# Kernel tuning notes

Hardware: AMD Instinct MI355X
Metric: run time of the kernel (lower is better)

## Reference

```python
import jax, jax.numpy as jnp
import numpy as np

N = 50000       # nodes
E = 800000      # edges (avg degree 16)
H = 64          # hidden_channels
T = 4           # towers
F = H // T      # per-tower channels (divide_input=True) = 16
NAGG, NSC = 5, 3
# degree histogram passed as mol_deg -> avg log-degree scaler constant (as in PyG PNAConv)
MOL_DEG = np.array([0, 5, 15, 30, 25, 15, 7, 2, 1], dtype=np.float64)
_bins = np.arange(len(MOL_DEG))
AVG_LOG = float((np.log(_bins + 1.0) * MOL_DEG).sum() / MOL_DEG.sum())


def setup_inputs() -> dict:
    key = jax.random.key(0)
    ks = jax.random.split(key, 12)
    g = lambda k, shp, s=0.1: jax.random.normal(k, shp, dtype=jnp.float32) * s
    return {
        "atom_x": g(ks[0], (N, H), 1.0),
        "bond_emb": g(ks[1], (5, H)),                      # Embedding(5, H)
        "edge_w": g(ks[2], (H, F)), "edge_b": jnp.zeros((F,), jnp.float32),
        "pre_w1": g(ks[3], (T, 3 * F, F)), "pre_b1": jnp.zeros((T, F), jnp.float32),
        "pre_w2": g(ks[4], (T, F, F)), "pre_b2": jnp.zeros((T, F), jnp.float32),
        "post_w1": g(ks[5], (T, (1 + NAGG * NSC) * F, F)), "post_b1": jnp.zeros((T, F), jnp.float32),
        "post_w2": g(ks[6], (T, F, F)), "post_b2": jnp.zeros((T, F), jnp.float32),
        "lin_w": g(ks[7], (H, H)), "lin_b": jnp.zeros((H,), jnp.float32),
        "ln_g": jnp.ones((H,), jnp.float32), "ln_b": jnp.zeros((H,), jnp.float32),
        "bond_x": jax.random.randint(ks[8], (E,), 0, 5),
        "atom_edge_index": jax.random.randint(ks[9], (2, E), 0, N),
    }


def reference(atom_x, bond_emb, edge_w, edge_b, pre_w1, pre_b1, pre_w2, pre_b2,
              post_w1, post_b1, post_w2, post_b2, lin_w, lin_b, ln_g, ln_b,
              bond_x, atom_edge_index):
    src, dst = atom_edge_index[0], atom_edge_index[1]
    # bond encoder + PNA edge encoder (edge_dim -> F_in)
    e = bond_emb[bond_x] @ edge_w + edge_b                       # [E, F]
    xt = atom_x.reshape(N, T, F)                                 # divide_input
    x_j, x_i = xt[src], xt[dst]                                  # [E, T, F]
    et = jnp.broadcast_to(e[:, None, :], (E, T, F))
    h = jnp.concatenate([x_i, x_j, et], axis=-1)                 # [E, T, 3F]
    # per-tower pre-MLP (Linear -> ReLU -> Linear)
    h = jax.nn.relu(jnp.einsum('etf,tfg->etg', h, pre_w1) + pre_b1)
    h = jnp.einsum('etf,tfg->etg', h, pre_w2) + pre_b2           # messages [E, T, F]

    s = jax.ops.segment_sum(h, dst, num_segments=N)
    cnt = jax.ops.segment_sum(jnp.ones((E,), h.dtype), dst, num_segments=N)
    cnt_c = jnp.maximum(cnt, 1.0)[:, None, None]
    mean = s / cnt_c
    mean2 = jax.ops.segment_sum(h * h, dst, num_segments=N) / cnt_c
    std = jnp.sqrt(jax.nn.relu(mean2 - mean * mean) + 1e-5)
    has = (cnt > 0)[:, None, None]
    mn = jnp.where(has, jax.ops.segment_min(h, dst, num_segments=N), 0.0)
    mx = jnp.where(has, jax.ops.segment_max(h, dst, num_segments=N), 0.0)
    agg = jnp.concatenate([s, mean, mn, mx, std], axis=-1)       # [N, T, 5F]

    # degree scalers (deg clamped to 1, as in PyG DegreeScalerAggregation)
    ld = jnp.log(jnp.maximum(cnt, 1.0) + 1.0)[:, None, None]
    agg = jnp.concatenate([agg, agg * (ld / AVG_LOG), agg * (AVG_LOG / ld)], axis=-1)  # [N, T, 15F]

    out = jnp.concatenate([xt, agg], axis=-1)                    # [N, T, 16F]
    # per-tower post-MLP, then mix towers with final Linear
    out = jax.nn.relu(jnp.einsum('ntf,tfg->ntg', out, post_w1) + post_b1)
    out = jnp.einsum('ntf,tfg->ntg', out, post_w2) + post_b2     # [N, T, F]
    out = out.reshape(N, H) @ lin_w + lin_b                      # [N, H]

    # LayerNorm + ReLU + residual (dropout is identity in eval)
    mu = out.mean(-1, keepdims=True)
    var = out.var(-1, keepdims=True)
    ln = (out - mu) / jnp.sqrt(var + 1e-5) * ln_g + ln_b
    return atom_x + jax.nn.relu(ln)
```

## Files before the change

### kernel.cpp

```cpp
#include <hip/hip_runtime.h>
#include <cstdint>

typedef unsigned short u16;
typedef _Float16 half4v __attribute__((ext_vector_type(4)));
typedef float f32x4 __attribute__((ext_vector_type(4)));

#define AVG_LOG_F 1.4862356961977451f
#define MAXD 64

#define OFF_W2   3072
#define OFF_PW1  4096
#define OFF_PW2  20480
#define OFF_LW   21504
#define OFF_PB1  25600
#define OFF_PB2  25664
#define OFF_QB1  25728
#define OFF_QB2  25792
#define OFF_LB   25856
#define OFF_LG   25920
#define OFF_LBN  25984
#define OFF_EWT  26128
#define IB       26448

__device__ __forceinline__ float bf2f(u16 u) {
    return __uint_as_float(((unsigned)u) << 16);
}
__device__ __forceinline__ u16 f2bf(float f) {
    unsigned u = __float_as_uint(f);
    u += 0x7fffu + ((u >> 16) & 1u);
    return (u16)(u >> 16);
}
__device__ __forceinline__ float rdin(const void* p, long j, int mode) {
    if (mode == 0) return bf2f(((const u16*)p)[j]);
    return ((const float*)p)[j];
}
template <int MODE>
__device__ __forceinline__ void load16c(const void* p, long base, float* o) {
    if (MODE == 0) {
        const u16* q = (const u16*)p + base;
        uint4 a = *(const uint4*)q;
        uint4 b = *(const uint4*)(q + 8);
        o[0]  = __uint_as_float(a.x << 16); o[1]  = __uint_as_float(a.x & 0xffff0000u);
        o[2]  = __uint_as_float(a.y << 16); o[3]  = __uint_as_float(a.y & 0xffff0000u);
        o[4]  = __uint_as_float(a.z << 16); o[5]  = __uint_as_float(a.z & 0xffff0000u);
        o[6]  = __uint_as_float(a.w << 16); o[7]  = __uint_as_float(a.w & 0xffff0000u);
        o[8]  = __uint_as_float(b.x << 16); o[9]  = __uint_as_float(b.x & 0xffff0000u);
        o[10] = __uint_as_float(b.y << 16); o[11] = __uint_as_float(b.y & 0xffff0000u);
        o[12] = __uint_as_float(b.z << 16); o[13] = __uint_as_float(b.z & 0xffff0000u);
        o[14] = __uint_as_float(b.w << 16); o[15] = __uint_as_float(b.w & 0xffff0000u);
    } else {
        const float* q = (const float*)p + base;
        float4 a = *(const float4*)q;
        float4 b = *(const float4*)(q + 4);
        float4 c = *(const float4*)(q + 8);
        float4 d = *(const float4*)(q + 12);
        o[0]=a.x; o[1]=a.y; o[2]=a.z; o[3]=a.w;
        o[4]=b.x; o[5]=b.y; o[6]=b.z; o[7]=b.w;
        o[8]=c.x; o[9]=c.y; o[10]=c.z; o[11]=c.w;
        o[12]=d.x; o[13]=d.y; o[14]=d.z; o[15]=d.w;
    }
}

template <int MODE>
__device__ __forceinline__ void y_loop(const void* ax, const void* pre_w1, float* wsY, float* wsXW,
                                       int Nn, int wave, int nwaves, int l) {
    const int t = l >> 4, g = l & 15;
    float wxi[16], wxj[16];
#pragma unroll
    for (int f = 0; f < 16; f++) {
        wxi[f] = rdin(pre_w1, t * 768 + f * 16 + g, MODE);
        wxj[f] = rdin(pre_w1, t * 768 + (16 + f) * 16 + g, MODE);
    }
    for (int n = wave; n < Nn; n += nwaves) {
        float xj[16];
        load16c<MODE>(ax, (long)n * 64 + t * 16, xj);
        float accY = 0.f, accX = 0.f;
#pragma unroll
        for (int f = 0; f < 16; f++) {
            accY = fmaf(xj[f], wxj[f], accY);
            accX = fmaf(xj[f], wxi[f], accX);
        }
        wsY[(long)n * 64 + l]  = accY;
        wsXW[(long)n * 64 + l] = accX;
    }
}

__global__ __launch_bounds__(256) void k_prep(
    const int* __restrict__ dstp, const int* __restrict__ srcp, const int* __restrict__ bondp,
    const void* bond_emb, const void* edge_w, const void* edge_b,
    const void* pre_w1, const void* pre_b1, const void* pre_w2, const void* pre_b2,
    const void* post_w1, const void* post_b1, const void* post_w2, const void* post_b2,
    const void* lin_w, const void* lin_b, const void* ln_g, const void* ln_b,
    const void* ax, float* wsf, float* wsY, float* wsXW,
    int* __restrict__ cnt, int* __restrict__ pk, int* modep,
    int Nn, int E, int NIB)
{
    int tid = threadIdx.x;
    if ((int)blockIdx.x >= NIB) {
        int e = ((int)blockIdx.x - NIB) * 256 + tid;
        if (e < E) {
            int d = dstp[e];
            int pos = atomicAdd(&cnt[d], 1);
            if (pos < MAXD) pk[d * MAXD + pos] = (srcp[e] << 9) | (bondp[e] & 7);
        }
        return;
    }
    __shared__ int csh;
    __shared__ float ET[80];
    if (tid == 0) csh = 0;
    __syncthreads();
    {
        unsigned v = ((const unsigned*)ax)[tid];
        unsigned lo = v & 0xffffu;
        int ee = (int)((lo >> 7) & 0xff);
        int isbf = (lo == 0u) || (ee >= 110 && ee <= 140);
        atomicAdd(&csh, isbf);
    }
    __syncthreads();
    int mode = (csh >= 192) ? 0 : 1;

    int b = (int)blockIdx.x;
    int gt = b * 256 + tid;
    int gs = NIB * 256;
    if (b == 0 && tid == 0) modep[0] = mode;

    for (int j = gt; j < 1024; j += gs)  wsf[OFF_W2 + j]  = rdin(pre_w2, j, mode);
    for (int j = gt; j < 16384; j += gs) wsf[OFF_PW1 + j] = rdin(post_w1, j, mode);
    for (int j = gt; j < 1024; j += gs)  wsf[OFF_PW2 + j] = rdin(post_w2, j, mode);
    for (int j = gt; j < 4096; j += gs)  wsf[OFF_LW + j]  = rdin(lin_w, j, mode);
    for (int j = gt; j < 64; j += gs) {
        wsf[OFF_PB1 + j] = rdin(pre_b1, j, mode);
        wsf[OFF_PB2 + j] = rdin(pre_b2, j, mode);
        wsf[OFF_QB1 + j] = rdin(post_b1, j, mode);
        wsf[OFF_QB2 + j] = rdin(post_b2, j, mode);
        wsf[OFF_LB + j]  = rdin(lin_b, j, mode);
        wsf[OFF_LG + j]  = rdin(ln_g, j, mode);
        wsf[OFF_LBN + j] = rdin(ln_b, j, mode);
    }
    if (b == 0) {
        if (tid < 80) {
            int bb = tid >> 4, f = tid & 15;
            float acc = rdin(edge_b, f, mode);
            for (int k = 0; k < 64; k++)
                acc = fmaf(rdin(bond_emb, bb * 64 + k, mode), rdin(edge_w, k * 16 + f, mode), acc);
            ET[tid] = acc;
        }
        __syncthreads();
        for (int j = tid; j < 320; j += 256) {
            int bb = j >> 6, ll = j & 63, tt = ll >> 4, gg = ll & 15;
            float acc = rdin(pre_b1, tt * 16 + gg, mode);
#pragma unroll
            for (int f = 0; f < 16; f++)
                acc = fmaf(ET[bb * 16 + f], rdin(pre_w1, tt * 768 + (32 + f) * 16 + gg, mode), acc);
            wsf[OFF_EWT + j] = acc;
        }
    }
    int wave = gt >> 6;
    int nwaves = gs >> 6;
    int l = tid & 63;
    if (mode == 0) y_loop<0>(ax, pre_w1, wsY, wsXW, Nn, wave, nwaves, l);
    else           y_loop<1>(ax, pre_w1, wsY, wsXW, Nn, wave, nwaves, l);
}

__global__ __launch_bounds__(256, 4) void k_node(
    const void* __restrict__ ax, const float* __restrict__ Yp, const float* __restrict__ XWp,
    const int* __restrict__ pk, const int* __restrict__ cnt,
    const float* __restrict__ wsf, void* __restrict__ outp,
    const int* __restrict__ modep, int Nn)
{
    __shared__ float hb[4][8][64];
    __shared__ _Float16 hbh[4][16][64];
    __shared__ float zws[4][5][64];
    __shared__ float qp[4][4][64];
    __shared__ float xrow[4][64];
    __shared__ float scl1s[4], scl2s[4];
    const int w = threadIdx.x >> 6;
    const int l = threadIdx.x & 63;
    const int t = l >> 4;
    const int g = l & 15;
    const int n = blockIdx.x * 4 + w;
    const int mode = modep[0];
    const bool active = (n < Nn);
    const int nn = active ? n : 0;

    const float* PW1 = wsf + OFF_PW1 + t * 4096;
    const float* PW2 = wsf + OFF_PW2 + t * 256;

    half4v bfr[4];
    float pb2a[4];
    {
        const int k4 = (l >> 4) << 2;
#pragma unroll
        for (int tt = 0; tt < 4; tt++) {
            half4v bv;
#pragma unroll
            for (int i = 0; i < 4; i++)
                bv[i] = (_Float16)wsf[OFF_W2 + tt * 256 + (k4 + i) * 16 + (l & 15)];
            bfr[tt] = bv;
            pb2a[tt] = wsf[OFF_PB2 + tt * 16 + (l & 15)];
        }
    }
    float qb1g = wsf[OFF_QB1 + t * 16 + g];
    float qb2g = wsf[OFF_QB2 + t * 16 + g];

    int deg = active ? cnt[nn] : 0;
    if (deg > MAXD) deg = MAXD;

    int   pkvAll = pk[nn * MAXD + l];
    float XWv    = XWp[(long)nn * 64 + l];
    zws[w][0][l] = XWv + wsf[OFF_EWT + 0 * 64 + l];
    zws[w][1][l] = XWv + wsf[OFF_EWT + 1 * 64 + l];
    zws[w][2][l] = XWv + wsf[OFF_EWT + 2 * 64 + l];
    zws[w][3][l] = XWv + wsf[OFF_EWT + 3 * 64 + l];
    zws[w][4][l] = XWv + wsf[OFF_EWT + 4 * 64 + l];
    xrow[w][l]   = rdin(ax, (long)nn * 64 + l, mode);

    float sA[4]  = {0.f, 0.f, 0.f, 0.f};
    float s2A[4] = {0.f, 0.f, 0.f, 0.f};
    float mnA[4] = {3.0e38f, 3.0e38f, 3.0e38f, 3.0e38f};
    float mxA[4] = {-3.0e38f, -3.0e38f, -3.0e38f, -3.0e38f};

    const _Float16* hrow = &hbh[w][l & 15][0];
    const int swz = (l & 7) << 3;
    const int aidx0 = (l >> 4) << 2;

    for (int kb = 0; kb < deg; kb += 16) {
        int B = deg - kb; if (B > 16) B = 16;
        int vs[16]; float yv[16];
#pragma unroll
        for (int k = 0; k < 16; k++) {
            if (k < B) {
                vs[k] = __builtin_amdgcn_readlane(pkvAll, kb + k);
                yv[k] = Yp[(vs[k] >> 3) + l];
            }
        }
#pragma unroll
        for (int k = 0; k < 16; k++) {
            float hv = (k < B) ? fmaxf(yv[k] + zws[w][vs[k] & 7][l], 0.f) : 0.f;
            hbh[w][k][l ^ ((k & 7) << 3)] = (_Float16)hv;
        }
        if (B == 16) {
#pragma unroll
            for (int tt = 0; tt < 4; tt++) {
                half4v a = *(const half4v*)&hrow[(tt * 16 + aidx0) ^ swz];
                f32x4 d = __builtin_amdgcn_mfma_f32_16x16x16f16(a, bfr[tt], (f32x4){0.f,0.f,0.f,0.f}, 0, 0, 0);
#pragma unroll
                for (int i = 0; i < 4; i++) {
                    float m = d[i] + pb2a[tt];
                    sA[tt] += m;
                    s2A[tt] = fmaf(m, m, s2A[tt]);
                    mnA[tt] = fminf(mnA[tt], m);
                    mxA[tt] = fmaxf(mxA[tt], m);
                }
            }
        } else {
            const int ebase = kb + aidx0;
#pragma unroll
            for (int tt = 0; tt < 4; tt++) {
                half4v a = *(const half4v*)&hrow[(tt * 16 + aidx0) ^ swz];
                f32x4 d = __builtin_amdgcn_mfma_f32_16x16x16f16(a, bfr[tt], (f32x4){0.f,0.f,0.f,0.f}, 0, 0, 0);
#pragma unroll
                for (int i = 0; i < 4; i++) {
                    bool val = (ebase + i) < deg;
                    float m = d[i] + pb2a[tt];
                    float mm = val ? m : 0.f;
                    sA[tt] += mm;
                    s2A[tt] = fmaf(mm, mm, s2A[tt]);
                    mnA[tt] = fminf(mnA[tt], val ? m : 3.0e38f);
                    mxA[tt] = fmaxf(mxA[tt], val ? m : -3.0e38f);
                }
            }
        }
    }

#pragma unroll
    for (int tt = 0; tt < 4; tt++) {
        sA[tt]  += __shfl_xor(sA[tt], 16);  sA[tt]  += __shfl_xor(sA[tt], 32);
        s2A[tt] += __shfl_xor(s2A[tt], 16); s2A[tt] += __shfl_xor(s2A[tt], 32);
        mnA[tt] = fminf(mnA[tt], __shfl_xor(mnA[tt], 16));
        mnA[tt] = fminf(mnA[tt], __shfl_xor(mnA[tt], 32));
        mxA[tt] = fmaxf(mxA[tt], __shfl_xor(mxA[tt], 16));
        mxA[tt] = fmaxf(mxA[tt], __shfl_xor(mxA[tt], 32));
    }
    float s  = (t & 2) ? ((t & 1) ? sA[3]  : sA[2])  : ((t & 1) ? sA[1]  : sA[0]);
    float s2 = (t & 2) ? ((t & 1) ? s2A[3] : s2A[2]) : ((t & 1) ? s2A[1] : s2A[0]);
    float mn = (t & 2) ? ((t & 1) ? mnA[3] : mnA[2]) : ((t & 1) ? mnA[1] : mnA[0]);
    float mx = (t & 2) ? ((t & 1) ? mxA[3] : mxA[2]) : ((t & 1) ? mxA[1] : mxA[0]);

    if (deg == 0) { mn = 0.f; mx = 0.f; }
    float cf = (float)(deg > 0 ? deg : 1);
    float inv = 1.0f / cf;
    float mean = s * inv;
    float var = s2 * inv - mean * mean;
    float sd = sqrtf(fmaxf(var, 0.f) + 1e-5f);
    float ldv = logf(cf + 1.0f);
    float sc1 = ldv * (1.0f / AVG_LOG_F);
    float sc2 = AVG_LOG_F / ldv;

    hb[w][0][l] = s;
    hb[w][1][l] = mean;
    hb[w][2][l] = mn;
    hb[w][3][l] = mx;
    hb[w][4][l] = sd;
    if (l == 0) { scl1s[w] = sc1; scl2s[w] = sc2; }
    __syncthreads();

    const int F0 = w * 4;
    float q0[4] = {0,0,0,0}, q1[4] = {0,0,0,0}, q2[4] = {0,0,0,0};
    {
        float xa[4][4];
#pragma unroll
        for (int nd = 0; nd < 4; nd++) {
            float4 v = *(const float4*)&xrow[nd][t * 16 + F0];
            xa[nd][0] = v.x; xa[nd][1] = v.y; xa[nd][2] = v.z; xa[nd][3] = v.w;
        }
#pragma unroll
        for (int fi = 0; fi < 4; fi++) {
            float wv = PW1[(F0 + fi) * 16 + g];
#pragma unroll
            for (int nd = 0; nd < 4; nd++) q0[nd] = fmaf(xa[nd][fi], wv, q0[nd]);
        }
    }
#pragma unroll
    for (int a = 0; a < 5; a++) {
        float xa[4][4];
#pragma unroll
        for (int nd = 0; nd < 4; nd++) {
            float4 v = *(const float4*)&hb[nd][a][t * 16 + F0];
            xa[nd][0] = v.x; xa[nd][1] = v.y; xa[nd][2] = v.z; xa[nd][3] = v.w;
        }
        const int rb = 16 + a * 16;
#pragma unroll
        for (int fi = 0; fi < 4; fi++) {
            const int r = (rb + F0 + fi) * 16 + g;
            float w0  = PW1[r];
            float w1  = PW1[r + 80 * 16];
            float w2v = PW1[r + 160 * 16];
#pragma unroll
            for (int nd = 0; nd < 4; nd++) {
                float x = xa[nd][fi];
                q0[nd] = fmaf(x, w0,  q0[nd]);
                q1[nd] = fmaf(x, w1,  q1[nd]);
                q2[nd] = fmaf(x, w2v, q2[nd]);
            }
        }
    }
#pragma unroll
    for (int nd = 0; nd < 4; nd++)
        qp[w][nd][l] = fmaf(scl2s[nd], q2[nd], fmaf(scl1s[nd], q1[nd], q0[nd]));
    __syncthreads();

    {
        float q0s = qp[0][w][l] + qp[1][w][l] + qp[2][w][l] + qp[3][w][l];
        float p1 = fmaxf(q0s + qb1g, 0.f);
        hb[w][5][l] = p1;
        float pw2c[16];
#pragma unroll
        for (int f = 0; f < 16; f++) pw2c[f] = PW2[f * 16 + g];
        float m2 = qb2g;
        const float4* pp = (const float4*)&hb[w][5][t * 16];
        float4 p0v = pp[0], r1 = pp[1], r2 = pp[2], r3 = pp[3];
        m2 = fmaf(p0v.x, pw2c[0],  m2); m2 = fmaf(p0v.y, pw2c[1],  m2);
        m2 = fmaf(p0v.z, pw2c[2],  m2); m2 = fmaf(p0v.w, pw2c[3],  m2);
        m2 = fmaf(r1.x, pw2c[4],  m2); m2 = fmaf(r1.y, pw2c[5],  m2);
        m2 = fmaf(r1.z, pw2c[6],  m2); m2 = fmaf(r1.w, pw2c[7],  m2);
        m2 = fmaf(r2.x, pw2c[8],  m2); m2 = fmaf(r2.y, pw2c[9],  m2);
        m2 = fmaf(r2.z, pw2c[10], m2); m2 = fmaf(r2.w, pw2c[11], m2);
        m2 = fmaf(r3.x, pw2c[12], m2); m2 = fmaf(r3.y, pw2c[13], m2);
        m2 = fmaf(r3.z, pw2c[14], m2); m2 = fmaf(r3.w, pw2c[15], m2);
        hb[w][6][l] = m2;
    }
    __syncthreads();

    {
        const float* LW = wsf + OFF_LW;
        const int fb = w * 16;
        float lw[4] = {0,0,0,0};
#pragma unroll
        for (int c = 0; c < 4; c++) {
            float pa[4][4];
#pragma unroll
            for (int nd = 0; nd < 4; nd++) {
                float4 v = *(const float4*)&hb[nd][6][fb + 4 * c];
                pa[nd][0] = v.x; pa[nd][1] = v.y; pa[nd][2] = v.z; pa[nd][3] = v.w;
            }
#pragma unroll
            for (int fi = 0; fi < 4; fi++) {
                float wl = LW[(fb + 4 * c + fi) * 64 + l];
#pragma unroll
                for (int nd = 0; nd < 4; nd++) lw[nd] = fmaf(pa[nd][fi], wl, lw[nd]);
            }
        }
#pragma unroll
        for (int nd = 0; nd < 4; nd++) qp[w][nd][l] = lw[nd];
    }
    __syncthreads();

    {
        float a = wsf[OFF_LB + l] + qp[0][w][l] + qp[1][w][l] + qp[2][w][l] + qp[3][w][l];
        float s1 = a, sq = a * a;
#pragma unroll
        for (int o = 1; o < 64; o <<= 1) { s1 += __shfl_xor(s1, o); sq += __shfl_xor(sq, o); }
        float mu = s1 * (1.0f / 64.0f);
        float varl = sq * (1.0f / 64.0f) - mu * mu;
        float ln = (a - mu) * rsqrtf(varl + 1e-5f) * wsf[OFF_LG + l] + wsf[OFF_LBN + l];
        if (active) {
            long idx = (long)n * 64 + l;
            float res = xrow[w][l] + fmaxf(ln, 0.f);
            if (mode == 0) ((u16*)outp)[idx] = f2bf(res);
            else           ((float*)outp)[idx] = res;
        }
    }
}

extern "C" void kernel_launch(void* const* d_in, const int* in_sizes, int n_in,
                              void* d_out, int out_size, void* d_ws, size_t ws_size,
                              hipStream_t stream) {
    const void* atom_x   = d_in[0];
    const void* bond_emb = d_in[1];
    const void* edge_w   = d_in[2];
    const void* edge_b   = d_in[3];
    const void* pre_w1   = d_in[4];
    const void* pre_b1   = d_in[5];
    const void* pre_w2   = d_in[6];
    const void* pre_b2   = d_in[7];
    const void* post_w1  = d_in[8];
    const void* post_b1  = d_in[9];
    const void* post_w2  = d_in[10];
    const void* post_b2  = d_in[11];
    const void* lin_w    = d_in[12];
    const void* lin_b    = d_in[13];
    const void* ln_g     = d_in[14];
    const void* ln_b     = d_in[15];
    const int* bond_x    = (const int*)d_in[16];
    const int* aei       = (const int*)d_in[17];

    int E  = in_sizes[16];
    int Nn = in_sizes[0] / 64;
    const int* srcp = aei;
    const int* dstp = aei + E;

    float* wsf = (float*)d_ws;
    int*   wsi = (int*)d_ws;

    size_t o = IB;
    int* modep = wsi + o; o += 16;
    int* cnt   = wsi + o; o += Nn;
    o = (o + 63) & ~(size_t)63;
    int* pk    = wsi + o; o += (size_t)Nn * MAXD;
    float* Yp  = (float*)(wsi + o); o += (size_t)Nn * 64;
    float* XWp = (float*)(wsi + o); o += (size_t)Nn * 64;

    const int NIB  = 1600;
    const int SBLK = (E + 255) / 256;

    (void)hipMemsetAsync(cnt, 0, (size_t)Nn * sizeof(int), stream);
    k_prep<<<NIB + SBLK, 256, 0, stream>>>(dstp, srcp, bond_x,
                                           bond_emb, edge_w, edge_b,
                                           pre_w1, pre_b1, pre_w2, pre_b2,
                                           post_w1, post_b1, post_w2, post_b2,
                                           lin_w, lin_b, ln_g, ln_b,
                                           atom_x, wsf, Yp, XWp, cnt, pk, modep, Nn, E, NIB);
    dim3 gn((Nn + 3) / 4, 1, 1);
    k_node<<<gn, 256, 0, stream>>>(atom_x, Yp, XWp, pk, cnt, wsf, d_out, modep, Nn);
}
```

Measured before the change: 289.2 us.

## Process 16 nodes per block and run node post-MLP and final linear on MFMA

Each block now handles 16 nodes, four per wave in sequence, instead of 4. This allows the per-tower post-MLP first and second layers and the tower-mixing linear layer to run as 16x16x16 fp16 MFMA tiles, replacing scalar FMA loops over shared memory. The aim is to amortise per-block weight loads and cut VALU work in the node epilogue. In exchange, the aggregates and intermediates are rounded to fp16, and the edge-aggregation phase per wave becomes serial over four nodes, which lowers block count and latency hiding.

```diff
diff --git a/kernel.cpp b/kernel.cpp
--- a/kernel.cpp
+++ b/kernel.cpp
@@ -168,245 +168,251 @@
     const float* __restrict__ wsf, void* __restrict__ outp,
     const int* __restrict__ modep, int Nn)
 {
-    __shared__ float hb[4][8][64];
     __shared__ _Float16 hbh[4][16][64];
-    __shared__ float zws[4][5][64];
-    __shared__ float qp[4][4][64];
-    __shared__ float xrow[4][64];
-    __shared__ float scl1s[4], scl2s[4];
+    __shared__ float    zws[4][5][64];
+    __shared__ _Float16 xih[16][64];
+    __shared__ _Float16 aggh[5][16][64];
+    __shared__ _Float16 p1h[16][64];
+    __shared__ _Float16 p2h[16][64];
+    __shared__ float    outf[16][64];
+    __shared__ float    scl1s[16], scl2s[16];
+
     const int w = threadIdx.x >> 6;
     const int l = threadIdx.x & 63;
-    const int t = l >> 4;
-    const int g = l & 15;
-    const int n = blockIdx.x * 4 + w;
     const int mode = modep[0];
-    const bool active = (n < Nn);
-    const int nn = active ? n : 0;
-
-    const float* PW1 = wsf + OFF_PW1 + t * 4096;
-    const float* PW2 = wsf + OFF_PW2 + t * 256;
+
+    const int col  = l & 15;
+    const int krow = (l >> 4) << 2;
 
     half4v bfr[4];
-    float pb2a[4];
-    {
-        const int k4 = (l >> 4) << 2;
-#pragma unroll
-        for (int tt = 0; tt < 4; tt++) {
-            half4v bv;
-#pragma unroll
-            for (int i = 0; i < 4; i++)
-                bv[i] = (_Float16)wsf[OFF_W2 + tt * 256 + (k4 + i) * 16 + (l & 15)];
-            bfr[tt] = bv;
-            pb2a[tt] = wsf[OFF_PB2 + tt * 16 + (l & 15)];
-        }
-    }
-    float qb1g = wsf[OFF_QB1 + t * 16 + g];
-    float qb2g = wsf[OFF_QB2 + t * 16 + g];
-
-    int deg = active ? cnt[nn] : 0;
-    if (deg > MAXD) deg = MAXD;
-
-    int   pkvAll = pk[nn * MAXD + l];
-    float XWv    = XWp[(long)nn * 64 + l];
-    zws[w][0][l] = XWv + wsf[OFF_EWT + 0 * 64 + l];
-    zws[w][1][l] = XWv + wsf[OFF_EWT + 1 * 64 + l];
-    zws[w][2][l] = XWv + wsf[OFF_EWT + 2 * 64 + l];
-    zws[w][3][l] = XWv + wsf[OFF_EWT + 3 * 64 + l];
-    zws[w][4][l] = XWv + wsf[OFF_EWT + 4 * 64 + l];
-    xrow[w][l]   = rdin(ax, (long)nn * 64 + l, mode);
-
-    float sA[4]  = {0.f, 0.f, 0.f, 0.f};
-    float s2A[4] = {0.f, 0.f, 0.f, 0.f};
-    float mnA[4] = {3.0e38f, 3.0e38f, 3.0e38f, 3.0e38f};
-    float mxA[4] = {-3.0e38f, -3.0e38f, -3.0e38f, -3.0e38f};
-
-    const _Float16* hrow = &hbh[w][l & 15][0];
-    const int swz = (l & 7) << 3;
-    const int aidx0 = (l >> 4) << 2;
-
-    for (int kb = 0; kb < deg; kb += 16) {
-        int B = deg - kb; if (B > 16) B = 16;
-        int vs[16]; float yv[16];
-#pragma unroll
-        for (int k = 0; k < 16; k++) {
-            if (k < B) {
-                vs[k] = __builtin_amdgcn_readlane(pkvAll, kb + k);
-                yv[k] = Yp[(vs[k] >> 3) + l];
-            }
-        }
-#pragma unroll
-        for (int k = 0; k < 16; k++) {
-            float hv = (k < B) ? fmaxf(yv[k] + zws[w][vs[k] & 7][l], 0.f) : 0.f;
-            hbh[w][k][l ^ ((k & 7) << 3)] = (_Float16)hv;
-        }
-        if (B == 16) {
-#pragma unroll
-            for (int tt = 0; tt < 4; tt++) {
-                half4v a = *(const half4v*)&hrow[(tt * 16 + aidx0) ^ swz];
-                f32x4 d = __builtin_amdgcn_mfma_f32_16x16x16f16(a, bfr[tt], (f32x4){0.f,0.f,0.f,0.f}, 0, 0, 0);
-#pragma unroll
-                for (int i = 0; i < 4; i++) {
-                    float m = d[i] + pb2a[tt];
-                    sA[tt] += m;
-                    s2A[tt] = fmaf(m, m, s2A[tt]);
-                    mnA[tt] = fminf(mnA[tt], m);
-                    mxA[tt] = fmaxf(mxA[tt], m);
+    f32x4 cinit[4];
+#pragma unroll
+    for (int tt = 0; tt < 4; tt++) {
+        half4v bv;
+#pragma unroll
+        for (int i = 0; i < 4; i++)
+            bv[i] = (_Float16)wsf[OFF_W2 + tt * 256 + (krow + i) * 16 + col];
+        bfr[tt] = bv;
+        float pb = wsf[OFF_PB2 + tt * 16 + col];
+        cinit[tt] = (f32x4){pb, pb, pb, pb};
+    }
+
+    const _Float16* hrow = &hbh[w][col][0];
+    const int eswz = (l & 7) << 3;
+
+    for (int j = 0; j < 4; j++) {
+        const int ndl = w * 4 + j;
+        const int ng  = blockIdx.x * 16 + ndl;
+        const bool act = (ng < Nn);
+        const int nn = act ? ng : 0;
+        int deg = act ? cnt[nn] : 0;
+        if (deg > MAXD) deg = MAXD;
+
+        int   pkv = pk[nn * MAXD + l];
+        float XWv = XWp[(long)nn * 64 + l];
+        zws[w][0][l] = XWv + wsf[OFF_EWT + 0 * 64 + l];
+        zws[w][1][l] = XWv + wsf[OFF_EWT + 1 * 64 + l];
+        zws[w][2][l] = XWv + wsf[OFF_EWT + 2 * 64 + l];
+        zws[w][3][l] = XWv + wsf[OFF_EWT + 3 * 64 + l];
+        zws[w][4][l] = XWv + wsf[OFF_EWT + 4 * 64 + l];
+        const int nsw = (ndl & 7) << 3;
+        xih[ndl][l ^ nsw] = (_Float16)rdin(ax, (long)nn * 64 + l, mode);
+
+        float sA[4]  = {0.f, 0.f, 0.f, 0.f};
+        float s2A[4] = {0.f, 0.f, 0.f, 0.f};
+        float mnA[4] = {3.0e38f, 3.0e38f, 3.0e38f, 3.0e38f};
+        float mxA[4] = {-3.0e38f, -3.0e38f, -3.0e38f, -3.0e38f};
+
+        for (int kb = 0; kb < deg; kb += 16) {
+            int B = deg - kb; if (B > 16) B = 16;
+            int vs[16]; float yv[16];
+#pragma unroll
+            for (int k = 0; k < 16; k++) {
+                if (k < B) {
+                    vs[k] = __builtin_amdgcn_readlane(pkv, kb + k);
+                    yv[k] = Yp[(vs[k] >> 3) + l];
                 }
             }
-        } else {
-            const int ebase = kb + aidx0;
-#pragma unroll
-            for (int tt = 0; tt < 4; tt++) {
-                half4v a = *(const half4v*)&hrow[(tt * 16 + aidx0) ^ swz];
-                f32x4 d = __builtin_amdgcn_mfma_f32_16x16x16f16(a, bfr[tt], (f32x4){0.f,0.f,0.f,0.f}, 0, 0, 0);
-#pragma unroll
-                for (int i = 0; i < 4; i++) {
-                    bool val = (ebase + i) < deg;
-                    float m = d[i] + pb2a[tt];
-                    float mm = val ? m : 0.f;
-                    sA[tt] += mm;
-                    s2A[tt] = fmaf(mm, mm, s2A[tt]);
-                    mnA[tt] = fminf(mnA[tt], val ? m : 3.0e38f);
-                    mxA[tt] = fmaxf(mxA[tt], val ? m : -3.0e38f);
+#pragma unroll
+            for (int k = 0; k < 16; k++) {
+                float hv = (k < B) ? fmaxf(yv[k] + zws[w][vs[k] & 7][l], 0.f) : 0.f;
+                hbh[w][k][l ^ ((k & 7) << 3)] = (_Float16)hv;
+            }
+            if (B == 16) {
+#pragma unroll
+                for (int tt = 0; tt < 4; tt++) {
+                    half4v a = *(const half4v*)&hrow[(tt * 16 + krow) ^ eswz];
+                    f32x4 d = __builtin_amdgcn_mfma_f32_16x16x16f16(a, bfr[tt], cinit[tt], 0, 0, 0);
+#pragma unroll
+                    for (int i = 0; i < 4; i++) {
+                        float m = d[i];
+                        sA[tt] += m;
+                        s2A[tt] = fmaf(m, m, s2A[tt]);
+                        mnA[tt] = fminf(mnA[tt], m);
+                        mxA[tt] = fmaxf(mxA[tt], m);
+                    }
+                }
+            } else {
+                const int ebase = kb + krow;
+#pragma unroll
+                for (int tt = 0; tt < 4; tt++) {
+                    half4v a = *(const half4v*)&hrow[(tt * 16 + krow) ^ eswz];
+                    f32x4 d = __builtin_amdgcn_mfma_f32_16x16x16f16(a, bfr[tt], cinit[tt], 0, 0, 0);
+#pragma unroll
+                    for (int i = 0; i < 4; i++) {
+                        bool val = (ebase + i) < deg;
+                        float m = d[i];
+                        float mm = val ? m : 0.f;
+                        sA[tt] += mm;
+                        s2A[tt] = fmaf(mm, mm, s2A[tt]);
+                        mnA[tt] = fminf(mnA[tt], val ? m : 3.0e38f);
+                        mxA[tt] = fmaxf(mxA[tt], val ? m : -3.0e38f);
+                    }
                 }
             }
         }
-    }
-
-#pragma unroll
-    for (int tt = 0; tt < 4; tt++) {
-        sA[tt]  += __shfl_xor(sA[tt], 16);  sA[tt]  += __shfl_xor(sA[tt], 32);
-        s2A[tt] += __shfl_xor(s2A[tt], 16); s2A[tt] += __shfl_xor(s2A[tt], 32);
-        mnA[tt] = fminf(mnA[tt], __shfl_xor(mnA[tt], 16));
-        mnA[tt] = fminf(mnA[tt], __shfl_xor(mnA[tt], 32));
-        mxA[tt] = fmaxf(mxA[tt], __shfl_xor(mxA[tt], 16));
-        mxA[tt] = fmaxf(mxA[tt], __shfl_xor(mxA[tt], 32));
-    }
-    float s  = (t & 2) ? ((t & 1) ? sA[3]  : sA[2])  : ((t & 1) ? sA[1]  : sA[0]);
-    float s2 = (t & 2) ? ((t & 1) ? s2A[3] : s2A[2]) : ((t & 1) ? s2A[1] : s2A[0]);
-    float mn = (t & 2) ? ((t & 1) ? mnA[3] : mnA[2]) : ((t & 1) ? mnA[1] : mnA[0]);
-    float mx = (t & 2) ? ((t & 1) ? mxA[3] : mxA[2]) : ((t & 1) ? mxA[1] : mxA[0]);
-
-    if (deg == 0) { mn = 0.f; mx = 0.f; }
-    float cf = (float)(deg > 0 ? deg : 1);
-    float inv = 1.0f / cf;
-    float mean = s * inv;
-    float var = s2 * inv - mean * mean;
-    float sd = sqrtf(fmaxf(var, 0.f) + 1e-5f);
-    float ldv = logf(cf + 1.0f);
-    float sc1 = ldv * (1.0f / AVG_LOG_F);
-    float sc2 = AVG_LOG_F / ldv;
-
-    hb[w][0][l] = s;
-    hb[w][1][l] = mean;
-    hb[w][2][l] = mn;
-    hb[w][3][l] = mx;
-    hb[w][4][l] = sd;
-    if (l == 0) { scl1s[w] = sc1; scl2s[w] = sc2; }
+
+#pragma unroll
+        for (int tt = 0; tt < 4; tt++) {
+            sA[tt]  += __shfl_xor(sA[tt], 16);  sA[tt]  += __shfl_xor(sA[tt], 32);
+            s2A[tt] += __shfl_xor(s2A[tt], 16); s2A[tt] += __shfl_xor(s2A[tt], 32);
+            mnA[tt] = fminf(mnA[tt], __shfl_xor(mnA[tt], 16));
+            mnA[tt] = fminf(mnA[tt], __shfl_xor(mnA[tt], 32));
+            mxA[tt] = fmaxf(mxA[tt], __shfl_xor(mxA[tt], 16));
+            mxA[tt] = fmaxf(mxA[tt], __shfl_xor(mxA[tt], 32));
+        }
+        const int t = l >> 4;
+        float s  = (t & 2) ? ((t & 1) ? sA[3]  : sA[2])  : ((t & 1) ? sA[1]  : sA[0]);
+        float s2 = (t & 2) ? ((t & 1) ? s2A[3] : s2A[2]) : ((t & 1) ? s2A[1] : s2A[0]);
+        float mn = (t & 2) ? ((t & 1) ? mnA[3] : mnA[2]) : ((t & 1) ? mnA[1] : mnA[0]);
+        float mx = (t & 2) ? ((t & 1) ? mxA[3] : mxA[2]) : ((t & 1) ? mxA[1] : mxA[0]);
+
+        if (deg == 0) { mn = 0.f; mx = 0.f; }
+        float cf = (float)(deg > 0 ? deg : 1);
+        float inv = 1.0f / cf;
+        float mean = s * inv;
+        float var = s2 * inv - mean * mean;
+        float sd = sqrtf(fmaxf(var, 0.f) + 1e-5f);
+        float ldv = logf(cf + 1.0f);
+
+        aggh[0][ndl][l ^ nsw] = (_Float16)s;
+        aggh[1][ndl][l ^ nsw] = (_Float16)mean;
+        aggh[2][ndl][l ^ nsw] = (_Float16)mn;
+        aggh[3][ndl][l ^ nsw] = (_Float16)mx;
+        aggh[4][ndl][l ^ nsw] = (_Float16)sd;
+        if (l == 0) {
+            scl1s[ndl] = ldv * (1.0f / AVG_LOG_F);
+            scl2s[ndl] = AVG_LOG_F / ldv;
+        }
+    }
     __syncthreads();
 
-    const int F0 = w * 4;
-    float q0[4] = {0,0,0,0}, q1[4] = {0,0,0,0}, q2[4] = {0,0,0,0};
+    const int t = w;
+    const float* PW1t = wsf + OFF_PW1 + t * 4096;
+    const int anode = col;
+    const int asw   = (anode & 7) << 3;
+    const int achan = t * 16 + krow;
+
+    half4v b1[16];
+#pragma unroll
+    for (int jj = 0; jj < 16; jj++) {
+        int rbase = (jj == 0) ? 0
+                  : (jj <= 5)  ? 16  + (jj - 1)  * 16
+                  : (jj <= 10) ? 96  + (jj - 6)  * 16
+                  :              176 + (jj - 11) * 16;
+        half4v bv;
+#pragma unroll
+        for (int i = 0; i < 4; i++)
+            bv[i] = (_Float16)PW1t[(rbase + krow + i) * 16 + col];
+        b1[jj] = bv;
+    }
+
+    f32x4 zero4 = (f32x4){0.f, 0.f, 0.f, 0.f};
+    f32x4 q0, q1v, q2v;
     {
-        float xa[4][4];
-#pragma unroll
-        for (int nd = 0; nd < 4; nd++) {
-            float4 v = *(const float4*)&xrow[nd][t * 16 + F0];
-            xa[nd][0] = v.x; xa[nd][1] = v.y; xa[nd][2] = v.z; xa[nd][3] = v.w;
-        }
-#pragma unroll
-        for (int fi = 0; fi < 4; fi++) {
-            float wv = PW1[(F0 + fi) * 16 + g];
-#pragma unroll
-            for (int nd = 0; nd < 4; nd++) q0[nd] = fmaf(xa[nd][fi], wv, q0[nd]);
-        }
-    }
-#pragma unroll
-    for (int a = 0; a < 5; a++) {
-        float xa[4][4];
-#pragma unroll
-        for (int nd = 0; nd < 4; nd++) {
-            float4 v = *(const float4*)&hb[nd][a][t * 16 + F0];
-            xa[nd][0] = v.x; xa[nd][1] = v.y; xa[nd][2] = v.z; xa[nd][3] = v.w;
-        }
-        const int rb = 16 + a * 16;
-#pragma unroll
-        for (int fi = 0; fi < 4; fi++) {
-            const int r = (rb + F0 + fi) * 16 + g;
-            float w0  = PW1[r];
-            float w1  = PW1[r + 80 * 16];
-            float w2v = PW1[r + 160 * 16];
-#pragma unroll
-            for (int nd = 0; nd < 4; nd++) {
-                float x = xa[nd][fi];
-                q0[nd] = fmaf(x, w0,  q0[nd]);
-                q1[nd] = fmaf(x, w1,  q1[nd]);
-                q2[nd] = fmaf(x, w2v, q2[nd]);
-            }
-        }
-    }
-#pragma unroll
-    for (int nd = 0; nd < 4; nd++)
-        qp[w][nd][l] = fmaf(scl2s[nd], q2[nd], fmaf(scl1s[nd], q1[nd], q0[nd]));
+        half4v a = *(const half4v*)&xih[anode][achan ^ asw];
+        q0 = __builtin_amdgcn_mfma_f32_16x16x16f16(a, b1[0], zero4, 0, 0, 0);
+    }
+#pragma unroll
+    for (int a5 = 0; a5 < 5; a5++) {
+        half4v a = *(const half4v*)&aggh[a5][anode][achan ^ asw];
+        q0 = __builtin_amdgcn_mfma_f32_16x16x16f16(a, b1[1 + a5], q0, 0, 0, 0);
+    }
+    q1v = zero4; q2v = zero4;
+#pragma unroll
+    for (int a5 = 0; a5 < 5; a5++) {
+        half4v a = *(const half4v*)&aggh[a5][anode][achan ^ asw];
+        q1v = __builtin_amdgcn_mfma_f32_16x16x16f16(a, b1[6 + a5],  q1v, 0, 0, 0);
+        q2v = __builtin_amdgcn_mfma_f32_16x16x16f16(a, b1[11 + a5], q2v, 0, 0, 0);
+    }
+    {
+        float qb1v = wsf[OFF_QB1 + t * 16 + col];
+#pragma unroll
+        for (int i = 0; i < 4; i++) {
+            int ndr = krow + i;
+            float p1 = q0[i] + scl1s[ndr] * q1v[i] + scl2s[ndr] * q2v[i] + qb1v;
+            p1 = fmaxf(p1, 0.f);
+            p1h[ndr][(t * 16 + col) ^ ((ndr & 7) << 3)] = (_Float16)p1;
+        }
+    }
+
+    {
+        const float* PW2t = wsf + OFF_PW2 + t * 256;
+        half4v b2;
+#pragma unroll
+        for (int i = 0; i < 4; i++)
+            b2[i] = (_Float16)PW2t[(krow + i) * 16 + col];
+        float qb2v = wsf[OFF_QB2 + t * 16 + col];
+        f32x4 c2 = (f32x4){qb2v, qb2v, qb2v, qb2v};
+        half4v a2 = *(const half4v*)&p1h[anode][achan ^ asw];
+        f32x4 m2 = __builtin_amdgcn_mfma_f32_16x16x16f16(a2, b2, c2, 0, 0, 0);
+#pragma unroll
+        for (int i = 0; i < 4; i++) {
+            int ndr = krow + i;
+            p2h[ndr][(t * 16 + col) ^ ((ndr & 7) << 3)] = (_Float16)m2[i];
+        }
+    }
     __syncthreads();
 
     {
-        float q0s = qp[0][w][l] + qp[1][w][l] + qp[2][w][l] + qp[3][w][l];
-        float p1 = fmaxf(q0s + qb1g, 0.f);
-        hb[w][5][l] = p1;
-        float pw2c[16];
-#pragma unroll
-        for (int f = 0; f < 16; f++) pw2c[f] = PW2[f * 16 + g];
-        float m2 = qb2g;
-        const float4* pp = (const float4*)&hb[w][5][t * 16];
-        float4 p0v = pp[0], r1 = pp[1], r2 = pp[2], r3 = pp[3];
-        m2 = fmaf(p0v.x, pw2c[0],  m2); m2 = fmaf(p0v.y, pw2c[1],  m2);
-        m2 = fmaf(p0v.z, pw2c[2],  m2); m2 = fmaf(p0v.w, pw2c[3],  m2);
-        m2 = fmaf(r1.x, pw2c[4],  m2); m2 = fmaf(r1.y, pw2c[5],  m2);
-        m2 = fmaf(r1.z, pw2c[6],  m2); m2 = fmaf(r1.w, pw2c[7],  m2);
-        m2 = fmaf(r2.x, pw2c[8],  m2); m2 = fmaf(r2.y, pw2c[9],  m2);
-        m2 = fmaf(r2.z, pw2c[10], m2); m2 = fmaf(r2.w, pw2c[11], m2);
-        m2 = fmaf(r3.x, pw2c[12], m2); m2 = fmaf(r3.y, pw2c[13], m2);
-        m2 = fmaf(r3.z, pw2c[14], m2); m2 = fmaf(r3.w, pw2c[15], m2);
-        hb[w][6][l] = m2;
+        const float* LWp = wsf + OFF_LW;
+        half4v bl[4];
+#pragma unroll
+        for (int s4 = 0; s4 < 4; s4++) {
+            half4v bv;
+#pragma unroll
+            for (int i = 0; i < 4; i++)
+                bv[i] = (_Float16)LWp[(16 * s4 + krow + i) * 64 + 16 * w + col];
+            bl[s4] = bv;
+        }
+        float lbv = wsf[OFF_LB + 16 * w + col];
+        f32x4 acc = (f32x4){lbv, lbv, lbv, lbv};
+#pragma unroll
+        for (int s4 = 0; s4 < 4; s4++) {
+            half4v a = *(const half4v*)&p2h[anode][(16 * s4 + krow) ^ asw];
+            acc = __builtin_amdgcn_mfma_f32_16x16x16f16(a, bl[s4], acc, 0, 0, 0);
+        }
+#pragma unroll
+        for (int i = 0; i < 4; i++) {
+            int ndr = krow + i;
+            outf[ndr][16 * w + col] = acc[i];
+        }
     }
     __syncthreads();
 
-    {
-        const float* LW = wsf + OFF_LW;
-        const int fb = w * 16;
-        float lw[4] = {0,0,0,0};
-#pragma unroll
-        for (int c = 0; c < 4; c++) {
-            float pa[4][4];
-#pragma unroll
-            for (int nd = 0; nd < 4; nd++) {
-                float4 v = *(const float4*)&hb[nd][6][fb + 4 * c];
-                pa[nd][0] = v.x; pa[nd][1] = v.y; pa[nd][2] = v.z; pa[nd][3] = v.w;
-            }
-#pragma unroll
-            for (int fi = 0; fi < 4; fi++) {
-                float wl = LW[(fb + 4 * c + fi) * 64 + l];
-#pragma unroll
-                for (int nd = 0; nd < 4; nd++) lw[nd] = fmaf(pa[nd][fi], wl, lw[nd]);
-            }
-        }
-#pragma unroll
-        for (int nd = 0; nd < 4; nd++) qp[w][nd][l] = lw[nd];
-    }
-    __syncthreads();
-
-    {
-        float a = wsf[OFF_LB + l] + qp[0][w][l] + qp[1][w][l] + qp[2][w][l] + qp[3][w][l];
+    for (int j = 0; j < 4; j++) {
+        const int ndl = w * 4 + j;
+        const int ng  = blockIdx.x * 16 + ndl;
+        float a = outf[ndl][l];
         float s1 = a, sq = a * a;
 #pragma unroll
         for (int o = 1; o < 64; o <<= 1) { s1 += __shfl_xor(s1, o); sq += __shfl_xor(sq, o); }
         float mu = s1 * (1.0f / 64.0f);
         float varl = sq * (1.0f / 64.0f) - mu * mu;
         float ln = (a - mu) * rsqrtf(varl + 1e-5f) * wsf[OFF_LG + l] + wsf[OFF_LBN + l];
-        if (active) {
-            long idx = (long)n * 64 + l;
-            float res = xrow[w][l] + fmaxf(ln, 0.f);
+        if (ng < Nn) {
+            long idx = (long)ng * 64 + l;
+            float res = rdin(ax, idx, mode) + fmaxf(ln, 0.f);
             if (mode == 0) ((u16*)outp)[idx] = f2bf(res);
             else           ((float*)outp)[idx] = res;
         }
@@ -461,6 +467,6 @@
                                            post_w1, post_b1, post_w2, post_b2,
                                            lin_w, lin_b, ln_g, ln_b,
                                            atom_x, wsf, Yp, XWp, cnt, pk, modep, Nn, E, NIB);
-    dim3 gn((Nn + 3) / 4, 1, 1);
+    dim3 gn((Nn + 15) / 16, 1, 1);
     k_node<<<gn, 256, 0, stream>>>(atom_x, Yp, XWp, pk, cnt, wsf, d_out, modep, Nn);
 }
```

Result: faster. 259.9 us (-10.1%).
